# Performance work log

Measured on AMD Instinct MI355X. Metric: run time of the kernel, lower is better.

Reference implementation:

```python
import jax, jax.numpy as jnp
import numpy as np
from jax import lax

B, T, V, E, H, C, K = 256, 512, 50000, 128, 256, 128, 2


def setup_inputs() -> dict:
    key = jax.random.key(0)
    ks = jax.random.split(key, 16)
    s = lambda *sh: 1.0 / np.sqrt(sh[0])
    return {
        "input_current": jax.random.randint(ks[0], (B, T), 0, V, dtype=jnp.int32),
        "input_left": jax.random.randint(ks[1], (B, T), 0, V, dtype=jnp.int32),
        "input_right": jax.random.randint(ks[2], (B, T), 0, V, dtype=jnp.int32),
        "emb": jax.random.normal(ks[3], (V, E), jnp.float32) * 0.05,
        "Wf": jax.random.normal(ks[4], (E, H), jnp.float32) * s(E),
        "Uf": jax.random.normal(ks[5], (H, H), jnp.float32) * s(H),
        "bf": jnp.zeros((H,), jnp.float32),
        "Wb": jax.random.normal(ks[6], (E, H), jnp.float32) * s(E),
        "Ub": jax.random.normal(ks[7], (H, H), jnp.float32) * s(H),
        "bb": jnp.zeros((H,), jnp.float32),
        "Wc": jax.random.normal(ks[8], (2 * H + E, C), jnp.float32) * s(2 * H + E),
        "bc": jnp.zeros((C,), jnp.float32),
        "Wd": jax.random.normal(ks[9], (C, K), jnp.float32) * s(C),
        "bd": jnp.zeros((K,), jnp.float32),
    }


def _simple_rnn(x, W, U, b):
    # x: [B,T,E] -> outputs [B,T,H]; h_t = tanh(x_t W + b + h_{t-1} U)
    xw = jnp.einsum("bte,eh->bth", x, W) + b  # precompute input projection
    h0 = jnp.zeros((x.shape[0], U.shape[0]), x.dtype)

    def step(h, xw_t):
        h = jnp.tanh(xw_t + h @ U)
        return h, h

    _, hs = lax.scan(step, h0, jnp.swapaxes(xw, 0, 1))  # scan over time
    return jnp.swapaxes(hs, 0, 1)


def reference(input_current, input_left, input_right, emb, Wf, Uf, bf, Wb, Ub, bb, Wc, bc, Wd, bd):
    e_cur = emb[input_current]  # [B,T,E]
    e_left = emb[input_left]
    e_right = emb[input_right]
    x_left = _simple_rnn(e_left, Wf, Uf, bf)  # [B,T,H]
    # go_backwards RNN: process reversed sequence, then model reverses back
    x_right = _simple_rnn(e_right[:, ::-1], Wb, Ub, bb)[:, ::-1]  # [B,T,H]
    x = jnp.concatenate([x_left, e_cur, x_right], axis=2)  # [B,T,2H+E]
    x = jnp.tanh(jnp.einsum("btd,dc->btc", x, Wc) + bc)  # Conv1D k=1 + tanh
    x = jnp.max(x, axis=1)  # GlobalMaxPooling1D
    return jax.nn.sigmoid(x @ Wd + bd)  # [B,K]
```

## Files before the change

kernel.cpp:

```cpp
#include <hip/hip_runtime.h>
#include <hip/hip_bf16.h>


#define B_ 256
#define T_ 512
#define E_ 128
#define H_ 256
#define C_ 128

typedef __attribute__((ext_vector_type(8))) short short8;
typedef __attribute__((ext_vector_type(4))) float float4v;
typedef __attribute__((ext_vector_type(2))) unsigned int uint2v;

__device__ inline unsigned short f2bf(float f) {
  unsigned u = __float_as_uint(f);
  u += 0x7fffu + ((u >> 16) & 1u);
  return (unsigned short)(u >> 16);
}
__device__ inline unsigned pkbf(float a, float b) {
  __hip_bfloat162 h2 = __float22bfloat162_rn(float2{a, b});
  union { __hip_bfloat162 h; unsigned u; } cv;
  cv.h = h2;
  return cv.u;
}
__device__ inline float lo16f(unsigned u) { return __uint_as_float(u << 16); }
__device__ inline float hi16f(unsigned u) { return __uint_as_float(u & 0xffff0000u); }
__device__ inline float fast_tanh(float x) {
  float e = __expf(2.f * x);
  float r = __builtin_amdgcn_rcpf(e + 1.f);
  return __builtin_fmaf(-2.f, r, 1.f);
}
__device__ inline unsigned enc_f(float f) {
  unsigned u = __float_as_uint(f);
  return (u & 0x80000000u) ? ~u : (u | 0x80000000u);
}
__device__ inline float dec_f(unsigned key) {
  unsigned bits = (key & 0x80000000u) ? (key ^ 0x80000000u) : ~key;
  return __uint_as_float(bits);
}
__device__ inline void sync_lds() {
  asm volatile("s_waitcnt lgkmcnt(0)\n\ts_barrier" ::: "memory");
}

__global__ __launch_bounds__(256) void prep_kernel(
    const float* __restrict__ Wf, const float* __restrict__ Wb,
    const float* __restrict__ Wc, const float* __restrict__ Uf,
    const float* __restrict__ Ub,
    unsigned short* __restrict__ WfT, unsigned short* __restrict__ WbT,
    unsigned short* __restrict__ WcT, unsigned short* __restrict__ UfT,
    unsigned short* __restrict__ UbT, unsigned int* __restrict__ pooled) {
  int gid = blockIdx.x * 256 + threadIdx.x;
  int stride = gridDim.x * 256;
  for (int i = gid; i < 128 * 256; i += stride) {
    int k = i >> 8, n = i & 255;
    WfT[n * 128 + k] = f2bf(Wf[i]);
    WbT[n * 128 + k] = f2bf(Wb[i]);
  }
  for (int i = gid; i < 640 * 128; i += stride) {
    int k = i >> 7, n = i & 127;
    WcT[n * 640 + k] = f2bf(Wc[i]);
  }
  for (int i = gid; i < 256 * 256; i += stride) {
    int k = i >> 8, n = i & 255;
    UfT[n * 256 + k] = f2bf(Uf[i]);
    UbT[n * 256 + k] = f2bf(Ub[i]);
  }
  for (int i = gid; i < B_ * C_; i += stride) pooled[i] = 0u;
}

__global__ __launch_bounds__(256) void embxw_kernel(
    const int* __restrict__ idxL, const int* __restrict__ idxR,
    const int* __restrict__ idxC, const float* __restrict__ emb,
    const unsigned short* __restrict__ WfT, const unsigned short* __restrict__ WbT,
    const float* __restrict__ bfv, const float* __restrict__ bbv,
    unsigned short* __restrict__ x) {
  const int dir = blockIdx.z;
  const int t0 = blockIdx.x * 8;
  const int b0 = blockIdx.y * 16;
  const int tid = threadIdx.x;
  const int w = tid >> 6, lane = tid & 63, q = lane >> 4, l15 = lane & 15;

  if (dir == 2) {
    const int tA = t0 + 2 * w, tB = tA + 1;
    const int erA = idxC[(b0 + l15) * T_ + tA];
    const int erB = idxC[(b0 + l15) * T_ + tB];
    const float* epA = emb + (size_t)erA * E_;
    const float* epB = emb + (size_t)erB * E_;
    float4v ga[8], gb[8];
#pragma unroll
    for (int u = 0; u < 8; ++u) ga[u] = *(const float4v*)(epA + 16 * u + 4 * q);
#pragma unroll
    for (int u = 0; u < 8; ++u) gb[u] = *(const float4v*)(epB + 16 * u + 4 * q);
#pragma unroll
    for (int u = 0; u < 8; ++u) {
      uint2v pk = {pkbf(ga[u][0], ga[u][1]), pkbf(ga[u][2], ga[u][3])};
      int row = b0 + u + 8 * (q >> 1);
      *(uint2v*)(x + ((size_t)row * T_ + tA) * 640 + 256 + 64 * (q & 1) +
                 4 * l15) = pk;
    }
#pragma unroll
    for (int u = 0; u < 8; ++u) {
      uint2v pk = {pkbf(gb[u][0], gb[u][1]), pkbf(gb[u][2], gb[u][3])};
      int row = b0 + u + 8 * (q >> 1);
      *(uint2v*)(x + ((size_t)row * T_ + tB) * 640 + 256 + 64 * (q & 1) +
                 4 * l15) = pk;
    }
    return;
  }

  const int* __restrict__ idx = dir ? idxR : idxL;
  const unsigned short* __restrict__ WT = dir ? WbT : WfT;
  const float* __restrict__ bias = dir ? bbv : bfv;

  short8 wfr[4][4];
#pragma unroll
  for (int mt = 0; mt < 4; ++mt)
#pragma unroll
    for (int kt = 0; kt < 4; ++kt)
      wfr[mt][kt] = *(const short8*)(WT + (64 * w + 16 * mt + l15) * 128 +
                                     kt * 32 + q * 8);
  float4v bv[4];
#pragma unroll
  for (int mt = 0; mt < 4; ++mt)
    bv[mt] = *(const float4v*)(bias + 64 * w + 16 * mt + 4 * q);

  int er[8];
#pragma unroll
  for (int j = 0; j < 8; ++j) er[j] = idx[(b0 + l15) * T_ + t0 + j];

  float4v g0[8], g1[8];
#pragma unroll
  for (int kt = 0; kt < 4; ++kt) {
    const float* p8 = emb + (size_t)er[0] * E_ + kt * 32 + q * 8;
    g0[2 * kt] = *(const float4v*)p8;
    g0[2 * kt + 1] = *(const float4v*)(p8 + 4);
  }
#pragma unroll
  for (int kt = 0; kt < 4; ++kt) {
    const float* p8 = emb + (size_t)er[1] * E_ + kt * 32 + q * 8;
    g1[2 * kt] = *(const float4v*)p8;
    g1[2 * kt + 1] = *(const float4v*)(p8 + 4);
  }

#pragma unroll 1
  for (int j = 0; j < 8; ++j) {
    float4v g2[8];
    if (j < 6) {
#pragma unroll
      for (int kt = 0; kt < 4; ++kt) {
        const float* p8 = emb + (size_t)er[j + 2] * E_ + kt * 32 + q * 8;
        g2[2 * kt] = *(const float4v*)p8;
        g2[2 * kt + 1] = *(const float4v*)(p8 + 4);
      }
    }
    short8 efr[4];
#pragma unroll
    for (int kt = 0; kt < 4; ++kt) {
      union { unsigned u[4]; short8 s; } cv;
      cv.u[0] = pkbf(g0[2 * kt][0], g0[2 * kt][1]);
      cv.u[1] = pkbf(g0[2 * kt][2], g0[2 * kt][3]);
      cv.u[2] = pkbf(g0[2 * kt + 1][0], g0[2 * kt + 1][1]);
      cv.u[3] = pkbf(g0[2 * kt + 1][2], g0[2 * kt + 1][3]);
      efr[kt] = cv.s;
    }
    float4v acc[4];
#pragma unroll
    for (int mt = 0; mt < 4; ++mt) acc[mt] = (float4v){0.f, 0.f, 0.f, 0.f};
#pragma unroll
    for (int kt = 0; kt < 4; ++kt)
#pragma unroll
      for (int mt = 0; mt < 4; ++mt)
        acc[mt] = __builtin_amdgcn_mfma_f32_16x16x32_bf16(wfr[mt][kt], efr[kt],
                                                          acc[mt], 0, 0, 0);
    const int t = t0 + j;
#pragma unroll
    for (int mt = 0; mt < 4; ++mt) {
      float4v v = acc[mt] + bv[mt];
      uint2v pk = {pkbf(v[0], v[1]), pkbf(v[2], v[3])};
      *(uint2v*)(x + ((size_t)(b0 + 4 * w + mt) * T_ + t) * 640 + dir * 384 +
                 lane * 4) = pk;
    }
#pragma unroll
    for (int kk = 0; kk < 8; ++kk) {
      g0[kk] = g1[kk];
      if (j < 6) g1[kk] = g2[kk];
    }
  }
}

__global__ __launch_bounds__(512, 2) void rnn_kernel(
    unsigned short* x, const unsigned short* __restrict__ UfT,
    const unsigned short* __restrict__ UbT) {
  const int dir = blockIdx.x & 1;
  const int b0 = (blockIdx.x >> 1) * 16;
  const unsigned short* __restrict__ UT = dir ? UbT : UfT;
  const int xoff = dir ? 384 : 0;
  const int tstep = dir ? -1 : 1;
  const int t0 = dir ? (T_ - 1) : 0;
  const ptrdiff_t dstep = (ptrdiff_t)tstep * 640;

  const int tid = threadIdx.x;
  const int wv = tid >> 6, lane = tid & 63, q = lane >> 4, l15 = lane & 15;

  __shared__ __attribute__((aligned(16))) unsigned short hbuf[2][16][280];
  unsigned short* hb0 = &hbuf[0][0][0];
  unsigned short* hb1 = &hbuf[1][0][0];

  for (int i = tid; i < 16 * 280; i += 512) hb0[i] = 0;

  short8 ufr[2][8];
#pragma unroll
  for (int mt = 0; mt < 2; ++mt)
#pragma unroll
    for (int kt = 0; kt < 8; ++kt)
      ufr[mt][kt] = *(const short8*)(UT + (32 * wv + 16 * mt + l15) * H_ +
                                     kt * 32 + q * 8);

  unsigned short* ptrS[2];
  const unsigned short* ptrL[2];
  uint2v curA[2], curB[2], infA[2], infB[2];
#pragma unroll
  for (int mt = 0; mt < 2; ++mt) {
    unsigned short* base =
        x + (size_t)(b0 + 2 * wv + mt) * T_ * 640 + xoff + lane * 4;
    unsigned short* bt = base + (ptrdiff_t)t0 * 640;
    curA[mt] = *(const uint2v*)(bt);
    curB[mt] = *(const uint2v*)(bt + dstep);
    infA[mt] = *(const uint2v*)(bt + 2 * dstep);
    infB[mt] = *(const uint2v*)(bt + 3 * dstep);
    ptrS[mt] = bt;
    ptrL[mt] = bt + 4 * dstep;
  }

  const unsigned lrd = l15 * 280;
  const unsigned lwr = l15 * 280 + 32 * wv;

  __syncthreads();

#pragma unroll 1
  for (int p = 0; p < 256; ++p) {
    uint2v ldA[2], ldB[2];
    if (p < 254) {
#pragma unroll
      for (int mt = 0; mt < 2; ++mt) {
        ldA[mt] = *(const uint2v*)(ptrL[mt]);
        ldB[mt] = *(const uint2v*)(ptrL[mt] + dstep);
      }
    } else {
#pragma unroll
      for (int mt = 0; mt < 2; ++mt) { ldA[mt] = infA[mt]; ldB[mt] = infB[mt]; }
    }
#pragma unroll
    for (int mt = 0; mt < 2; ++mt) ptrL[mt] += 2 * dstep;

    {
      short8 afr[8];
#pragma unroll
      for (int kt = 0; kt < 8; ++kt)
        afr[kt] = *(const short8*)(hb0 + lrd + kt * 32 + q * 8);
      float4v acc[2];
#pragma unroll
      for (int mt = 0; mt < 2; ++mt)
        acc[mt] = (float4v){lo16f(curA[mt].x), hi16f(curA[mt].x),
                            lo16f(curA[mt].y), hi16f(curA[mt].y)};
#pragma unroll
      for (int kt = 0; kt < 8; ++kt)
#pragma unroll
        for (int mt = 0; mt < 2; ++mt)
          acc[mt] = __builtin_amdgcn_mfma_f32_16x16x32_bf16(
              ufr[mt][kt], afr[kt], acc[mt], 0, 0, 0);
#pragma unroll
      for (int mt = 0; mt < 2; ++mt) {
        uint2v hv = {pkbf(fast_tanh(acc[mt][0]), fast_tanh(acc[mt][1])),
                     pkbf(fast_tanh(acc[mt][2]), fast_tanh(acc[mt][3]))};
        *(uint2v*)(hb1 + lwr + 16 * mt + 4 * q) = hv;
        *(uint2v*)ptrS[mt] = hv;
      }
    }
    sync_lds();

    {
      short8 afr[8];
#pragma unroll
      for (int kt = 0; kt < 8; ++kt)
        afr[kt] = *(const short8*)(hb1 + lrd + kt * 32 + q * 8);
      float4v acc[2];
#pragma unroll
      for (int mt = 0; mt < 2; ++mt)
        acc[mt] = (float4v){lo16f(curB[mt].x), hi16f(curB[mt].x),
                            lo16f(curB[mt].y), hi16f(curB[mt].y)};
#pragma unroll
      for (int kt = 0; kt < 8; ++kt)
#pragma unroll
        for (int mt = 0; mt < 2; ++mt)
          acc[mt] = __builtin_amdgcn_mfma_f32_16x16x32_bf16(
              ufr[mt][kt], afr[kt], acc[mt], 0, 0, 0);
#pragma unroll
      for (int mt = 0; mt < 2; ++mt) {
        uint2v hv = {pkbf(fast_tanh(acc[mt][0]), fast_tanh(acc[mt][1])),
                     pkbf(fast_tanh(acc[mt][2]), fast_tanh(acc[mt][3]))};
        *(uint2v*)(hb0 + lwr + 16 * mt + 4 * q) = hv;
        *(uint2v*)(ptrS[mt] + dstep) = hv;
      }
    }
#pragma unroll
    for (int mt = 0; mt < 2; ++mt) {
      ptrS[mt] += 2 * dstep;
      curA[mt] = infA[mt];
      curB[mt] = infB[mt];
      infA[mt] = ldA[mt];
      infB[mt] = ldB[mt];
    }
    sync_lds();
  }
}

__global__ __launch_bounds__(256, 2) void convpool_kernel(
    const unsigned short* __restrict__ x, const unsigned short* __restrict__ WcT,
    const float* __restrict__ bc, unsigned int* __restrict__ pooled) {
  const int b0 = (blockIdx.x & 15) * 16;
  const int t0 = (blockIdx.x >> 4) * 16;
  const int tid = threadIdx.x;
  const int w = tid >> 6, lane = tid & 63, q = lane >> 4, l15 = lane & 15;

  __shared__ __attribute__((aligned(16))) unsigned short tile[2][16][648];

  short8 wfr[2][20];
#pragma unroll
  for (int ct = 0; ct < 2; ++ct)
#pragma unroll
    for (int kt = 0; kt < 20; ++kt)
      wfr[ct][kt] = *(const short8*)(WcT +
                                     (size_t)(32 * w + 16 * ct + l15) * 640 +
                                     kt * 32 + q * 8);
  float4v bv[2];
#pragma unroll
  for (int ct = 0; ct < 2; ++ct)
    bv[ct] = *(const float4v*)(bc + 32 * w + 16 * ct + 4 * q);

  float4v mx[2];
  mx[0] = (float4v){-1e30f, -1e30f, -1e30f, -1e30f};
  mx[1] = mx[0];

  const int srow = tid >> 4, ssub = tid & 15;
  {
    const unsigned short* src = x + ((size_t)(b0 + srow) * T_ + t0) * 640;
#pragma unroll
    for (int j = 0; j < 5; ++j)
      *(short8*)&tile[0][srow][ssub * 8 + j * 128] =
          *(const short8*)(src + ssub * 8 + j * 128);
  }
  __syncthreads();

#pragma unroll 1
  for (int j = 0; j < 16; ++j) {
    const int t = t0 + j;
    const int buf = j & 1;
    if (j < 15) {
      const unsigned short* src = x + ((size_t)(b0 + srow) * T_ + t + 1) * 640;
#pragma unroll
      for (int jj = 0; jj < 5; ++jj)
        *(short8*)&tile[buf ^ 1][srow][ssub * 8 + jj * 128] =
            *(const short8*)(src + ssub * 8 + jj * 128);
    }
    float4v acc[2];
    acc[0] = (float4v){0.f, 0.f, 0.f, 0.f};
    acc[1] = (float4v){0.f, 0.f, 0.f, 0.f};
#pragma unroll
    for (int kt = 0; kt < 20; ++kt) {
      int row, so1, so2;
      if (kt < 8) {
        row = 2 * kt + (q >> 1);
        so1 = 64 * (2 * (q & 1)) + 4 * l15;
        so2 = so1 + 64;
      } else if (kt < 12) {
        row = 2 * (kt - 8) + (q >> 1) + 8 * (q & 1);
        so1 = 256 + 4 * l15;
        so2 = 320 + 4 * l15;
      } else {
        row = 2 * (kt - 12) + (q >> 1);
        so1 = 384 + 64 * (2 * (q & 1)) + 4 * l15;
        so2 = so1 + 64;
      }
      union { unsigned u[4]; short8 s; } cv;
      uint2v c1 = *(const uint2v*)&tile[buf][row][so1];
      uint2v c2 = *(const uint2v*)&tile[buf][row][so2];
      cv.u[0] = c1.x; cv.u[1] = c1.y; cv.u[2] = c2.x; cv.u[3] = c2.y;
      acc[0] = __builtin_amdgcn_mfma_f32_16x16x32_bf16(wfr[0][kt], cv.s,
                                                       acc[0], 0, 0, 0);
      acc[1] = __builtin_amdgcn_mfma_f32_16x16x32_bf16(wfr[1][kt], cv.s,
                                                       acc[1], 0, 0, 0);
    }
#pragma unroll
    for (int ct = 0; ct < 2; ++ct)
#pragma unroll
      for (int i = 0; i < 4; ++i)
        mx[ct][i] = fmaxf(mx[ct][i], acc[ct][i]);
    __syncthreads();
  }
#pragma unroll
  for (int ct = 0; ct < 2; ++ct)
#pragma unroll
    for (int i = 0; i < 4; ++i)
      atomicMax(pooled + (b0 + l15) * C_ + 32 * w + 16 * ct + 4 * q + i,
                enc_f(fast_tanh(mx[ct][i] + bv[ct][i])));
}

__global__ __launch_bounds__(256) void dense_kernel(
    const unsigned int* __restrict__ pooled, const float* __restrict__ Wd,
    const float* __restrict__ bd, float* __restrict__ out) {
  int b = threadIdx.x;
  float s0 = bd[0], s1 = bd[1];
#pragma unroll 4
  for (int c = 0; c < C_; ++c) {
    float f = dec_f(pooled[b * C_ + c]);
    s0 += f * Wd[c * 2 + 0];
    s1 += f * Wd[c * 2 + 1];
  }
  out[b * 2 + 0] = 1.f / (1.f + __expf(-s0));
  out[b * 2 + 1] = 1.f / (1.f + __expf(-s1));
}

extern "C" void kernel_launch(void* const* d_in, const int* in_sizes, int n_in,
                              void* d_out, int out_size, void* d_ws, size_t ws_size,
                              hipStream_t stream) {
  const int* idxC = (const int*)d_in[0];
  const int* idxL = (const int*)d_in[1];
  const int* idxR = (const int*)d_in[2];
  const float* emb = (const float*)d_in[3];
  const float* Wf = (const float*)d_in[4];
  const float* Uf = (const float*)d_in[5];
  const float* bf_ = (const float*)d_in[6];
  const float* Wb = (const float*)d_in[7];
  const float* Ub = (const float*)d_in[8];
  const float* bb_ = (const float*)d_in[9];
  const float* Wc = (const float*)d_in[10];
  const float* bc = (const float*)d_in[11];
  const float* Wd = (const float*)d_in[12];
  const float* bd = (const float*)d_in[13];

  char* ws = (char*)d_ws;
  unsigned short* x = (unsigned short*)ws;
  unsigned int* pooled = (unsigned int*)(ws + 167772160);
  unsigned short* WfT = (unsigned short*)(ws + 167772160 + 131072);
  unsigned short* WbT = WfT + 256 * 128;
  unsigned short* WcT = WbT + 256 * 128;
  unsigned short* UfT = WcT + 128 * 640;
  unsigned short* UbT = UfT + 256 * 256;

  prep_kernel<<<64, 256, 0, stream>>>(Wf, Wb, Wc, Uf, Ub, WfT, WbT, WcT, UfT,
                                      UbT, pooled);
  embxw_kernel<<<dim3(64, 16, 3), 256, 0, stream>>>(idxL, idxR, idxC, emb,
                                                    WfT, WbT, bf_, bb_, x);
  rnn_kernel<<<32, 512, 0, stream>>>(x, UfT, UbT);
  convpool_kernel<<<512, 256, 0, stream>>>(x, WcT, bc, pooled);
  dense_kernel<<<1, 256, 0, stream>>>(pooled, Wd, bd, (float*)d_out);
}
```

Baseline: 607.1 us.

## Fuse embedding projection into RNN kernel with flag-based producer-consumer overlap

Merges the embedding gather/input-projection kernel and the RNN kernel into one launch. The first 32 blocks run the recurrence and spin on per-chunk global flags, while the other blocks produce input projections in time order and publish flags with release semantics. The goal is to hide the projection phase behind the serial recurrence instead of running them back to back. It requests 120KB of dynamic shared memory so only one block fits per CU, and it depends on the 32 RNN blocks being resident alongside the producer blocks to avoid deadlock.

```diff
diff --git a/kernel.cpp b/kernel.cpp
--- a/kernel.cpp
+++ b/kernel.cpp
@@ -41,6 +41,16 @@
 __device__ inline void sync_lds() {
   asm volatile("s_waitcnt lgkmcnt(0)\n\ts_barrier" ::: "memory");
 }
+__device__ inline int clampt(int t) { return t < 0 ? 0 : (t > 511 ? 511 : t); }
+
+__device__ inline void wait_flag(const int* f) {
+  if (__hip_atomic_load(f, __ATOMIC_RELAXED, __HIP_MEMORY_SCOPE_AGENT) == 0) {
+    while (__hip_atomic_load(f, __ATOMIC_RELAXED, __HIP_MEMORY_SCOPE_AGENT) ==
+           0)
+      __builtin_amdgcn_s_sleep(8);
+  }
+  (void)__hip_atomic_load(f, __ATOMIC_ACQUIRE, __HIP_MEMORY_SCOPE_AGENT);
+}
 
 __global__ __launch_bounds__(256) void prep_kernel(
     const float* __restrict__ Wf, const float* __restrict__ Wb,
@@ -48,7 +58,8 @@
     const float* __restrict__ Ub,
     unsigned short* __restrict__ WfT, unsigned short* __restrict__ WbT,
     unsigned short* __restrict__ WcT, unsigned short* __restrict__ UfT,
-    unsigned short* __restrict__ UbT, unsigned int* __restrict__ pooled) {
+    unsigned short* __restrict__ UbT, unsigned int* __restrict__ pooled,
+    int* __restrict__ flags) {
   int gid = blockIdx.x * 256 + threadIdx.x;
   int stride = gridDim.x * 256;
   for (int i = gid; i < 128 * 256; i += stride) {
@@ -66,22 +77,255 @@
     UbT[n * 256 + k] = f2bf(Ub[i]);
   }
   for (int i = gid; i < B_ * C_; i += stride) pooled[i] = 0u;
-}
-
-__global__ __launch_bounds__(256) void embxw_kernel(
+  for (int i = gid; i < 1024; i += stride) flags[i] = 0;
+}
+
+__global__ __launch_bounds__(512, 1) void fused_kernel(
     const int* __restrict__ idxL, const int* __restrict__ idxR,
     const int* __restrict__ idxC, const float* __restrict__ emb,
-    const unsigned short* __restrict__ WfT, const unsigned short* __restrict__ WbT,
+    const unsigned short* __restrict__ WfT,
+    const unsigned short* __restrict__ WbT,
     const float* __restrict__ bfv, const float* __restrict__ bbv,
-    unsigned short* __restrict__ x) {
-  const int dir = blockIdx.z;
-  const int t0 = blockIdx.x * 8;
-  const int b0 = blockIdx.y * 16;
+    const unsigned short* __restrict__ UfT,
+    const unsigned short* __restrict__ UbT, unsigned short* x,
+    int* __restrict__ flags) {
+  const int blk = blockIdx.x;
   const int tid = threadIdx.x;
-  const int w = tid >> 6, lane = tid & 63, q = lane >> 4, l15 = lane & 15;
-
-  if (dir == 2) {
-    const int tA = t0 + 2 * w, tB = tA + 1;
+  const int lane = tid & 63, q = lane >> 4, l15 = lane & 15;
+
+  __shared__ __attribute__((aligned(16))) unsigned short hbuf[2][16][280];
+
+  if (blk < 32) {
+    const int dir = blk & 1;
+    const int btile = blk >> 1;
+    const int b0 = btile * 16;
+    const unsigned short* __restrict__ UT = dir ? UbT : UfT;
+    const int xoff = dir ? 384 : 0;
+    const int tstep = dir ? -1 : 1;
+    const int t0 = dir ? (T_ - 1) : 0;
+    const ptrdiff_t dstep = (ptrdiff_t)tstep * 640;
+    const int wv = tid >> 6;
+    const int* fl = flags + (dir * 16 + btile) * 32;
+
+    unsigned short* hb0 = &hbuf[0][0][0];
+    unsigned short* hb1 = &hbuf[1][0][0];
+    for (int i = tid; i < 16 * 280; i += 512) hb0[i] = 0;
+
+    short8 ufr[2][8];
+#pragma unroll
+    for (int mt = 0; mt < 2; ++mt)
+#pragma unroll
+      for (int kt = 0; kt < 8; ++kt)
+        ufr[mt][kt] = *(const short8*)(UT + (32 * wv + 16 * mt + l15) * H_ +
+                                       kt * 32 + q * 8);
+
+    int lastc = dir ? 31 : 0;
+    wait_flag(fl + lastc);
+
+    unsigned short* ptrS[2];
+    const unsigned short* ptrL[2];
+    uint2v curA[2], curB[2], infA[2], infB[2];
+#pragma unroll
+    for (int mt = 0; mt < 2; ++mt) {
+      unsigned short* base =
+          x + (size_t)(b0 + 2 * wv + mt) * T_ * 640 + xoff + lane * 4;
+      unsigned short* bt = base + (ptrdiff_t)t0 * 640;
+      curA[mt] = *(const uint2v*)(bt);
+      curB[mt] = *(const uint2v*)(bt + dstep);
+      infA[mt] = *(const uint2v*)(bt + 2 * dstep);
+      infB[mt] = *(const uint2v*)(bt + 3 * dstep);
+      ptrS[mt] = bt;
+      ptrL[mt] = bt + 4 * dstep;
+    }
+
+    const unsigned lrd = l15 * 280;
+    const unsigned lwr = l15 * 280 + 32 * wv;
+
+    __syncthreads();
+
+#pragma unroll 1
+    for (int p = 0; p < 256; ++p) {
+      int c = dir ? ((506 - 2 * p) >> 4) : ((2 * p + 5) >> 4);
+      c = c < 0 ? 0 : (c > 31 ? 31 : c);
+      if (c != lastc) {
+        wait_flag(fl + c);
+        lastc = c;
+      }
+      uint2v ldA[2], ldB[2];
+      if (p < 254) {
+#pragma unroll
+        for (int mt = 0; mt < 2; ++mt) {
+          ldA[mt] = *(const uint2v*)(ptrL[mt]);
+          ldB[mt] = *(const uint2v*)(ptrL[mt] + dstep);
+        }
+      } else {
+#pragma unroll
+        for (int mt = 0; mt < 2; ++mt) {
+          ldA[mt] = infA[mt];
+          ldB[mt] = infB[mt];
+        }
+      }
+#pragma unroll
+      for (int mt = 0; mt < 2; ++mt) ptrL[mt] += 2 * dstep;
+
+      {
+        short8 afr[8];
+#pragma unroll
+        for (int kt = 0; kt < 8; ++kt)
+          afr[kt] = *(const short8*)(hb0 + lrd + kt * 32 + q * 8);
+        float4v acc[2];
+#pragma unroll
+        for (int mt = 0; mt < 2; ++mt)
+          acc[mt] = (float4v){lo16f(curA[mt].x), hi16f(curA[mt].x),
+                              lo16f(curA[mt].y), hi16f(curA[mt].y)};
+#pragma unroll
+        for (int kt = 0; kt < 8; ++kt)
+#pragma unroll
+          for (int mt = 0; mt < 2; ++mt)
+            acc[mt] = __builtin_amdgcn_mfma_f32_16x16x32_bf16(
+                ufr[mt][kt], afr[kt], acc[mt], 0, 0, 0);
+#pragma unroll
+        for (int mt = 0; mt < 2; ++mt) {
+          uint2v hv = {pkbf(fast_tanh(acc[mt][0]), fast_tanh(acc[mt][1])),
+                       pkbf(fast_tanh(acc[mt][2]), fast_tanh(acc[mt][3]))};
+          *(uint2v*)(hb1 + lwr + 16 * mt + 4 * q) = hv;
+          *(uint2v*)ptrS[mt] = hv;
+        }
+      }
+      sync_lds();
+
+      {
+        short8 afr[8];
+#pragma unroll
+        for (int kt = 0; kt < 8; ++kt)
+          afr[kt] = *(const short8*)(hb1 + lrd + kt * 32 + q * 8);
+        float4v acc[2];
+#pragma unroll
+        for (int mt = 0; mt < 2; ++mt)
+          acc[mt] = (float4v){lo16f(curB[mt].x), hi16f(curB[mt].x),
+                              lo16f(curB[mt].y), hi16f(curB[mt].y)};
+#pragma unroll
+        for (int kt = 0; kt < 8; ++kt)
+#pragma unroll
+          for (int mt = 0; mt < 2; ++mt)
+            acc[mt] = __builtin_amdgcn_mfma_f32_16x16x32_bf16(
+                ufr[mt][kt], afr[kt], acc[mt], 0, 0, 0);
+#pragma unroll
+        for (int mt = 0; mt < 2; ++mt) {
+          uint2v hv = {pkbf(fast_tanh(acc[mt][0]), fast_tanh(acc[mt][1])),
+                       pkbf(fast_tanh(acc[mt][2]), fast_tanh(acc[mt][3]))};
+          *(uint2v*)(hb0 + lwr + 16 * mt + 4 * q) = hv;
+          *(uint2v*)(ptrS[mt] + dstep) = hv;
+        }
+      }
+#pragma unroll
+      for (int mt = 0; mt < 2; ++mt) {
+        ptrS[mt] += 2 * dstep;
+        curA[mt] = infA[mt];
+        curB[mt] = infB[mt];
+        infA[mt] = ldA[mt];
+        infB[mt] = ldB[mt];
+      }
+      sync_lds();
+    }
+    return;
+  }
+
+  if (blk < 1056) {
+    const int b2 = blk - 32;
+    const int z = b2 >> 5, r = b2 & 31;
+    const int btile = r & 15, dirg = r >> 4;
+    const int chunk = dirg ? (31 - z) : z;
+    const int w8 = tid >> 6;
+    const int g = w8 >> 2, wv = w8 & 3;
+    const int t0 = chunk * 16 + g * 8;
+    const int b0 = btile * 16;
+    const int* __restrict__ idx = dirg ? idxR : idxL;
+    const unsigned short* __restrict__ WT = dirg ? WbT : WfT;
+    const float* __restrict__ bias = dirg ? bbv : bfv;
+
+    short8 wfr[4][4];
+#pragma unroll
+    for (int mt = 0; mt < 4; ++mt)
+#pragma unroll
+      for (int kt = 0; kt < 4; ++kt)
+        wfr[mt][kt] = *(const short8*)(WT + (64 * wv + 16 * mt + l15) * 128 +
+                                       kt * 32 + q * 8);
+    float4v bv[4];
+#pragma unroll
+    for (int mt = 0; mt < 4; ++mt)
+      bv[mt] = *(const float4v*)(bias + 64 * wv + 16 * mt + 4 * q);
+
+    int er[8];
+#pragma unroll
+    for (int j = 0; j < 8; ++j) er[j] = idx[(b0 + l15) * T_ + t0 + j];
+
+    float4v g0[8];
+#pragma unroll
+    for (int kt = 0; kt < 4; ++kt) {
+      const float* p8 = emb + (size_t)er[0] * E_ + kt * 32 + q * 8;
+      g0[2 * kt] = *(const float4v*)p8;
+      g0[2 * kt + 1] = *(const float4v*)(p8 + 4);
+    }
+
+#pragma unroll 1
+    for (int j = 0; j < 8; ++j) {
+      float4v gn[8];
+      if (j < 7) {
+#pragma unroll
+        for (int kt = 0; kt < 4; ++kt) {
+          const float* p8 = emb + (size_t)er[j + 1] * E_ + kt * 32 + q * 8;
+          gn[2 * kt] = *(const float4v*)p8;
+          gn[2 * kt + 1] = *(const float4v*)(p8 + 4);
+        }
+      }
+      short8 efr[4];
+#pragma unroll
+      for (int kt = 0; kt < 4; ++kt) {
+        union { unsigned u[4]; short8 s; } cv;
+        cv.u[0] = pkbf(g0[2 * kt][0], g0[2 * kt][1]);
+        cv.u[1] = pkbf(g0[2 * kt][2], g0[2 * kt][3]);
+        cv.u[2] = pkbf(g0[2 * kt + 1][0], g0[2 * kt + 1][1]);
+        cv.u[3] = pkbf(g0[2 * kt + 1][2], g0[2 * kt + 1][3]);
+        efr[kt] = cv.s;
+      }
+      float4v acc[4];
+#pragma unroll
+      for (int mt = 0; mt < 4; ++mt) acc[mt] = (float4v){0.f, 0.f, 0.f, 0.f};
+#pragma unroll
+      for (int kt = 0; kt < 4; ++kt)
+#pragma unroll
+        for (int mt = 0; mt < 4; ++mt)
+          acc[mt] = __builtin_amdgcn_mfma_f32_16x16x32_bf16(
+              wfr[mt][kt], efr[kt], acc[mt], 0, 0, 0);
+      const int t = t0 + j;
+#pragma unroll
+      for (int mt = 0; mt < 4; ++mt) {
+        float4v v = acc[mt] + bv[mt];
+        uint2v pk = {pkbf(v[0], v[1]), pkbf(v[2], v[3])};
+        *(uint2v*)(x + ((size_t)(b0 + 4 * wv + mt) * T_ + t) * 640 +
+                   dirg * 384 + lane * 4) = pk;
+      }
+      if (j < 7) {
+#pragma unroll
+        for (int kk = 0; kk < 8; ++kk) g0[kk] = gn[kk];
+      }
+    }
+    __syncthreads();
+    if (tid == 0) {
+      __threadfence();
+      __hip_atomic_store(flags + (dirg * 16 + btile) * 32 + chunk, 1,
+                         __ATOMIC_RELEASE, __HIP_MEMORY_SCOPE_AGENT);
+    }
+    return;
+  }
+
+  {
+    const int b3 = blk - 1056;
+    const int btile = b3 & 15, tch = b3 >> 4;
+    const int b0 = btile * 16;
+    const int w8 = tid >> 6;
+    const int tA = tch * 16 + 2 * w8, tB = tA + 1;
     const int erA = idxC[(b0 + l15) * T_ + tA];
     const int erB = idxC[(b0 + l15) * T_ + tB];
     const float* epA = emb + (size_t)erA * E_;
@@ -105,213 +349,6 @@
       *(uint2v*)(x + ((size_t)row * T_ + tB) * 640 + 256 + 64 * (q & 1) +
                  4 * l15) = pk;
     }
-    return;
-  }
-
-  const int* __restrict__ idx = dir ? idxR : idxL;
-  const unsigned short* __restrict__ WT = dir ? WbT : WfT;
-  const float* __restrict__ bias = dir ? bbv : bfv;
-
-  short8 wfr[4][4];
-#pragma unroll
-  for (int mt = 0; mt < 4; ++mt)
-#pragma unroll
-    for (int kt = 0; kt < 4; ++kt)
-      wfr[mt][kt] = *(const short8*)(WT + (64 * w + 16 * mt + l15) * 128 +
-                                     kt * 32 + q * 8);
-  float4v bv[4];
-#pragma unroll
-  for (int mt = 0; mt < 4; ++mt)
-    bv[mt] = *(const float4v*)(bias + 64 * w + 16 * mt + 4 * q);
-
-  int er[8];
-#pragma unroll
-  for (int j = 0; j < 8; ++j) er[j] = idx[(b0 + l15) * T_ + t0 + j];
-
-  float4v g0[8], g1[8];
-#pragma unroll
-  for (int kt = 0; kt < 4; ++kt) {
-    const float* p8 = emb + (size_t)er[0] * E_ + kt * 32 + q * 8;
-    g0[2 * kt] = *(const float4v*)p8;
-    g0[2 * kt + 1] = *(const float4v*)(p8 + 4);
-  }
-#pragma unroll
-  for (int kt = 0; kt < 4; ++kt) {
-    const float* p8 = emb + (size_t)er[1] * E_ + kt * 32 + q * 8;
-    g1[2 * kt] = *(const float4v*)p8;
-    g1[2 * kt + 1] = *(const float4v*)(p8 + 4);
-  }
-
-#pragma unroll 1
-  for (int j = 0; j < 8; ++j) {
-    float4v g2[8];
-    if (j < 6) {
-#pragma unroll
-      for (int kt = 0; kt < 4; ++kt) {
-        const float* p8 = emb + (size_t)er[j + 2] * E_ + kt * 32 + q * 8;
-        g2[2 * kt] = *(const float4v*)p8;
-        g2[2 * kt + 1] = *(const float4v*)(p8 + 4);
-      }
-    }
-    short8 efr[4];
-#pragma unroll
-    for (int kt = 0; kt < 4; ++kt) {
-      union { unsigned u[4]; short8 s; } cv;
-      cv.u[0] = pkbf(g0[2 * kt][0], g0[2 * kt][1]);
-      cv.u[1] = pkbf(g0[2 * kt][2], g0[2 * kt][3]);
-      cv.u[2] = pkbf(g0[2 * kt + 1][0], g0[2 * kt + 1][1]);
-      cv.u[3] = pkbf(g0[2 * kt + 1][2], g0[2 * kt + 1][3]);
-      efr[kt] = cv.s;
-    }
-    float4v acc[4];
-#pragma unroll
-    for (int mt = 0; mt < 4; ++mt) acc[mt] = (float4v){0.f, 0.f, 0.f, 0.f};
-#pragma unroll
-    for (int kt = 0; kt < 4; ++kt)
-#pragma unroll
-      for (int mt = 0; mt < 4; ++mt)
-        acc[mt] = __builtin_amdgcn_mfma_f32_16x16x32_bf16(wfr[mt][kt], efr[kt],
-                                                          acc[mt], 0, 0, 0);
-    const int t = t0 + j;
-#pragma unroll
-    for (int mt = 0; mt < 4; ++mt) {
-      float4v v = acc[mt] + bv[mt];
-      uint2v pk = {pkbf(v[0], v[1]), pkbf(v[2], v[3])};
-      *(uint2v*)(x + ((size_t)(b0 + 4 * w + mt) * T_ + t) * 640 + dir * 384 +
-                 lane * 4) = pk;
-    }
-#pragma unroll
-    for (int kk = 0; kk < 8; ++kk) {
-      g0[kk] = g1[kk];
-      if (j < 6) g1[kk] = g2[kk];
-    }
-  }
-}
-
-__global__ __launch_bounds__(512, 2) void rnn_kernel(
-    unsigned short* x, const unsigned short* __restrict__ UfT,
-    const unsigned short* __restrict__ UbT) {
-  const int dir = blockIdx.x & 1;
-  const int b0 = (blockIdx.x >> 1) * 16;
-  const unsigned short* __restrict__ UT = dir ? UbT : UfT;
-  const int xoff = dir ? 384 : 0;
-  const int tstep = dir ? -1 : 1;
-  const int t0 = dir ? (T_ - 1) : 0;
-  const ptrdiff_t dstep = (ptrdiff_t)tstep * 640;
-
-  const int tid = threadIdx.x;
-  const int wv = tid >> 6, lane = tid & 63, q = lane >> 4, l15 = lane & 15;
-
-  __shared__ __attribute__((aligned(16))) unsigned short hbuf[2][16][280];
-  unsigned short* hb0 = &hbuf[0][0][0];
-  unsigned short* hb1 = &hbuf[1][0][0];
-
-  for (int i = tid; i < 16 * 280; i += 512) hb0[i] = 0;
-
-  short8 ufr[2][8];
-#pragma unroll
-  for (int mt = 0; mt < 2; ++mt)
-#pragma unroll
-    for (int kt = 0; kt < 8; ++kt)
-      ufr[mt][kt] = *(const short8*)(UT + (32 * wv + 16 * mt + l15) * H_ +
-                                     kt * 32 + q * 8);
-
-  unsigned short* ptrS[2];
-  const unsigned short* ptrL[2];
-  uint2v curA[2], curB[2], infA[2], infB[2];
-#pragma unroll
-  for (int mt = 0; mt < 2; ++mt) {
-    unsigned short* base =
-        x + (size_t)(b0 + 2 * wv + mt) * T_ * 640 + xoff + lane * 4;
-    unsigned short* bt = base + (ptrdiff_t)t0 * 640;
-    curA[mt] = *(const uint2v*)(bt);
-    curB[mt] = *(const uint2v*)(bt + dstep);
-    infA[mt] = *(const uint2v*)(bt + 2 * dstep);
-    infB[mt] = *(const uint2v*)(bt + 3 * dstep);
-    ptrS[mt] = bt;
-    ptrL[mt] = bt + 4 * dstep;
-  }
-
-  const unsigned lrd = l15 * 280;
-  const unsigned lwr = l15 * 280 + 32 * wv;
-
-  __syncthreads();
-
-#pragma unroll 1
-  for (int p = 0; p < 256; ++p) {
-    uint2v ldA[2], ldB[2];
-    if (p < 254) {
-#pragma unroll
-      for (int mt = 0; mt < 2; ++mt) {
-        ldA[mt] = *(const uint2v*)(ptrL[mt]);
-        ldB[mt] = *(const uint2v*)(ptrL[mt] + dstep);
-      }
-    } else {
-#pragma unroll
-      for (int mt = 0; mt < 2; ++mt) { ldA[mt] = infA[mt]; ldB[mt] = infB[mt]; }
-    }
-#pragma unroll
-    for (int mt = 0; mt < 2; ++mt) ptrL[mt] += 2 * dstep;
-
-    {
-      short8 afr[8];
-#pragma unroll
-      for (int kt = 0; kt < 8; ++kt)
-        afr[kt] = *(const short8*)(hb0 + lrd + kt * 32 + q * 8);
-      float4v acc[2];
-#pragma unroll
-      for (int mt = 0; mt < 2; ++mt)
-        acc[mt] = (float4v){lo16f(curA[mt].x), hi16f(curA[mt].x),
-                            lo16f(curA[mt].y), hi16f(curA[mt].y)};
-#pragma unroll
-      for (int kt = 0; kt < 8; ++kt)
-#pragma unroll
-        for (int mt = 0; mt < 2; ++mt)
-          acc[mt] = __builtin_amdgcn_mfma_f32_16x16x32_bf16(
-              ufr[mt][kt], afr[kt], acc[mt], 0, 0, 0);
-#pragma unroll
-      for (int mt = 0; mt < 2; ++mt) {
-        uint2v hv = {pkbf(fast_tanh(acc[mt][0]), fast_tanh(acc[mt][1])),
-                     pkbf(fast_tanh(acc[mt][2]), fast_tanh(acc[mt][3]))};
-        *(uint2v*)(hb1 + lwr + 16 * mt + 4 * q) = hv;
-        *(uint2v*)ptrS[mt] = hv;
-      }
-    }
-    sync_lds();
-
-    {
-      short8 afr[8];
-#pragma unroll
-      for (int kt = 0; kt < 8; ++kt)
-        afr[kt] = *(const short8*)(hb1 + lrd + kt * 32 + q * 8);
-      float4v acc[2];
-#pragma unroll
-      for (int mt = 0; mt < 2; ++mt)
-        acc[mt] = (float4v){lo16f(curB[mt].x), hi16f(curB[mt].x),
-                            lo16f(curB[mt].y), hi16f(curB[mt].y)};
-#pragma unroll
-      for (int kt = 0; kt < 8; ++kt)
-#pragma unroll
-        for (int mt = 0; mt < 2; ++mt)
-          acc[mt] = __builtin_amdgcn_mfma_f32_16x16x32_bf16(
-              ufr[mt][kt], afr[kt], acc[mt], 0, 0, 0);
-#pragma unroll
-      for (int mt = 0; mt < 2; ++mt) {
-        uint2v hv = {pkbf(fast_tanh(acc[mt][0]), fast_tanh(acc[mt][1])),
-                     pkbf(fast_tanh(acc[mt][2]), fast_tanh(acc[mt][3]))};
-        *(uint2v*)(hb0 + lwr + 16 * mt + 4 * q) = hv;
-        *(uint2v*)(ptrS[mt] + dstep) = hv;
-      }
-    }
-#pragma unroll
-    for (int mt = 0; mt < 2; ++mt) {
-      ptrS[mt] += 2 * dstep;
-      curA[mt] = infA[mt];
-      curB[mt] = infB[mt];
-      infA[mt] = ldA[mt];
-      infB[mt] = ldB[mt];
-    }
-    sync_lds();
   }
 }
 
@@ -442,17 +479,18 @@
   char* ws = (char*)d_ws;
   unsigned short* x = (unsigned short*)ws;
   unsigned int* pooled = (unsigned int*)(ws + 167772160);
-  unsigned short* WfT = (unsigned short*)(ws + 167772160 + 131072);
+  unsigned short* WfT = (unsigned short*)(ws + 167903232);
   unsigned short* WbT = WfT + 256 * 128;
   unsigned short* WcT = WbT + 256 * 128;
   unsigned short* UfT = WcT + 128 * 640;
   unsigned short* UbT = UfT + 256 * 256;
+  int* flags = (int*)(ws + 168460288);
 
   prep_kernel<<<64, 256, 0, stream>>>(Wf, Wb, Wc, Uf, Ub, WfT, WbT, WcT, UfT,
-                                      UbT, pooled);
-  embxw_kernel<<<dim3(64, 16, 3), 256, 0, stream>>>(idxL, idxR, idxC, emb,
-                                                    WfT, WbT, bf_, bb_, x);
-  rnn_kernel<<<32, 512, 0, stream>>>(x, UfT, UbT);
+                                      UbT, pooled, flags);
+  fused_kernel<<<1568, 512, 120 * 1024, stream>>>(idxL, idxR, idxC, emb, WfT,
+                                                  WbT, bf_, bb_, UfT, UbT, x,
+                                                  flags);
   convpool_kernel<<<512, 256, 0, stream>>>(x, WcT, bc, pooled);
   dense_kernel<<<1, 256, 0, stream>>>(pooled, Wd, bd, (float*)d_out);
 }
```

After: 589.5 us. 1.03x faster.
